# Performance work log

Hardware: AMD Instinct MI355X
Metric: run time of the kernel (lower is better)

The kernel has to match this reference:

```python
import jax, jax.numpy as jnp
import numpy as np

EPS_LN = 1e-6
EPS_STAT = 1e-10
EPS_BN = 1e-5


def _ln(x, g, b):
    mu = x.mean(-1, keepdims=True)
    var = x.var(-1, keepdims=True)
    return (x - mu) * jax.lax.rsqrt(var + EPS_LN) * g + b


def setup_inputs() -> dict:
    key = jax.random.key(0)
    ks = jax.random.split(key, 16)
    B, D, L, NB = 64, 256, 2048, 2
    H = 2 * D  # FFN inner dim
    s = 0.05   # small init scale for stability
    f32 = jnp.float32
    return {
        "x": jax.random.normal(ks[0], (B, D, L), f32),
        "wk": jax.random.normal(ks[1], (NB, 128, D), f32) * s,
        "wq": jax.random.normal(ks[2], (NB, 128, 2 * D), f32) * s,
        "fcq_w": jax.random.normal(ks[3], (NB, D, D), f32) * s,
        "fc_w": jax.random.normal(ks[4], (NB, D, 2 * D), f32) * s,
        "fc_b": jax.random.normal(ks[5], (NB, D), f32) * s,
        "att_ln_g": jnp.ones((NB, D), f32),
        "att_ln_b": jnp.zeros((NB, D), f32),
        "w1": jax.random.normal(ks[6], (NB, H, D), f32) * s,
        "b1": jax.random.normal(ks[7], (NB, H), f32) * s,
        "w2": jax.random.normal(ks[8], (NB, D, H), f32) * s,
        "b2": jax.random.normal(ks[9], (NB, D), f32) * s,
        "ffw_ln_g": jnp.ones((NB, D), f32),
        "ffw_ln_b": jnp.zeros((NB, D), f32),
    }


def reference(x, wk, wq, fcq_w, fc_w, fc_b, att_ln_g, att_ln_b,
              w1, b1, w2, b2, ffw_ln_g, ffw_ln_b):
    # x: (B, D, L)
    n_blocks = wk.shape[0]
    scale = 1.0 / np.sqrt(128.0)  # dim = k channel dim = 128
    v = x
    skip_sum = None
    for i in range(n_blocks):
        residual = v                                   # (B, D, L)
        vt = _ln(v.transpose(0, 2, 1), att_ln_g[i], att_ln_b[i])  # (B, L, D)
        k = jnp.einsum('bld,kd->blk', vt, wk[i])       # (B, L, 128)
        mu = vt.mean(axis=1, keepdims=True)            # (B, 1, D)
        sd = jnp.sqrt(jnp.clip(vt.var(axis=1, keepdims=True), EPS_STAT, None))
        q = jnp.einsum('bhe,ke->bhk',
                       jnp.concatenate([mu, sd], axis=2), wq[i])  # (B, 1, 128)
        scores = jnp.einsum('blk,bhk->bhl', k, q) * scale         # (B, 1, L)
        w = jax.nn.softmax(scores, axis=2)
        vdl = vt.transpose(0, 2, 1)                    # (B, D, L)
        att_mean = jnp.einsum('bdl,bhl->bdh', vdl, w)  # (B, D, 1)
        att_std = jnp.sqrt(jnp.clip(
            jnp.einsum('bdl,bhl->bdh', (vdl - att_mean) ** 2, w), EPS_STAT, None))
        skip = jnp.einsum('od,bdh->boh', fc_w[i],
                          jnp.concatenate([att_mean, att_std], axis=1)) \
               + fc_b[i][None, :, None]                # (B, D, 1)
        q_out = residual + jnp.einsum('od,bdh->boh', fcq_w[i], att_mean)  # (B, D, L)
        # PositionwiseFeedForward on (B, L, D)
        f_in = q_out.transpose(0, 2, 1)
        h = _ln(f_in, ffw_ln_g[i], ffw_ln_b[i])
        h1 = jax.nn.relu(jnp.einsum('bld,hd->blh', h, w1[i]) + b1[i])
        h2 = jnp.einsum('blh,dh->bld', h1, w2[i]) + b2[i]
        v = (h2 + f_in).transpose(0, 2, 1)             # (B, D, L)
        skip_sum = skip if skip_sum is None else skip_sum + skip
    # relu + BatchNorm1d (affine=False, training-mode batch stats)
    y = jax.nn.relu(skip_sum)                          # (B, D, 1)
    bm = y.mean(axis=(0, 2), keepdims=True)
    bv = y.var(axis=(0, 2), keepdims=True)
    return (y - bm) * jax.lax.rsqrt(bv + EPS_BN)
```

## Files before the change

kernel.cpp:

```cpp
#include <hip/hip_runtime.h>
#include <hip/hip_bf16.h>

#define DEV __device__ __forceinline__

constexpr int B = 64, D = 256, L = 2048, H = 512, KP = 128;
constexpr float EPS_LN = 1e-6f, EPS_STAT = 1e-10f, EPS_BN = 1e-5f;
constexpr float SCALE = 0.088388347648318447f;

typedef __attribute__((ext_vector_type(8))) short short8;
typedef __attribute__((ext_vector_type(4))) float float4_;
typedef __attribute__((ext_vector_type(2))) float float2_;

DEV unsigned short f2bf(float x) {
  unsigned u = __builtin_bit_cast(unsigned, x);
  u += 0x7fffu + ((u >> 16) & 1u);
  return (unsigned short)(u >> 16);
}

DEV unsigned pk2bf(float a, float b) {
  return (unsigned)f2bf(a) | ((unsigned)f2bf(b) << 16);
}

DEV float wred(float x) {
  #pragma unroll
  for (int o = 32; o > 0; o >>= 1) x += __shfl_down(x, o, 64);
  return x;
}
DEV float wredmax(float x) {
  #pragma unroll
  for (int o = 32; o > 0; o >>= 1) x = fmaxf(x, __shfl_down(x, o, 64));
  return x;
}

__global__ void k_convw(const float* __restrict__ w1, const float* __restrict__ w2,
                        unsigned short* __restrict__ w1b, unsigned short* __restrict__ w2b) {
  int n = H * D;
  for (int i = blockIdx.x * blockDim.x + threadIdx.x; i < n; i += gridDim.x * blockDim.x) {
    w1b[i] = f2bf(w1[i]);
    w2b[i] = f2bf(w2[i]);
  }
}

__global__ __launch_bounds__(512, 4) void k_pass1(
    const float* __restrict__ v, float* __restrict__ m, float* __restrict__ r,
    float* __restrict__ S1p, float* __restrict__ S2p) {
  __shared__ float ut[256 * 65];
  __shared__ float mu_s[64], rs_s[64];
  float* part1 = ut;
  float* part2 = ut + 2048;

  int blk = blockIdx.x;
  int b = blk >> 5, tile = blk & 31, l0 = tile * 64;
  int tid = threadIdx.x;
  int lane4 = tid & 15, rg = tid >> 4;

  const float* vrow = v + ((size_t)b * D + rg * 8) * L + l0 + lane4 * 4;
  float4_ vv[8];
  float4_ s1 = {0.f, 0.f, 0.f, 0.f}, s2 = {0.f, 0.f, 0.f, 0.f};
  #pragma unroll
  for (int j = 0; j < 8; ++j) {
    float4_ x = *(const float4_*)&vrow[(size_t)j * L];
    vv[j] = x; s1 += x; s2 += x * x;
  }
  #pragma unroll
  for (int c = 0; c < 4; ++c) {
    part1[rg * 64 + lane4 * 4 + c] = s1[c];
    part2[rg * 64 + lane4 * 4 + c] = s2[c];
  }
  __syncthreads();
  if (tid < 64) {
    float a = 0.f, c = 0.f;
    #pragma unroll
    for (int q = 0; q < 32; ++q) { a += part1[q * 64 + tid]; c += part2[q * 64 + tid]; }
    float mu = a * (1.f / D);
    float var = c * (1.f / D) - mu * mu;
    float rsq = rsqrtf(var + EPS_LN);
    mu_s[tid] = mu; rs_s[tid] = rsq;
    m[b * L + l0 + tid] = mu;
    r[b * L + l0 + tid] = rsq;
  }
  __syncthreads();
  {
    #pragma unroll
    for (int c = 0; c < 4; ++c) {
      int tok = lane4 * 4 + c;
      float mu = mu_s[tok], rsv = rs_s[tok];
      #pragma unroll
      for (int j = 0; j < 8; ++j)
        ut[(rg * 8 + j) * 65 + tok] = (vv[j][c] - mu) * rsv;
    }
  }
  __syncthreads();
  {
    int d = tid >> 1, hf = (tid & 1) * 32;
    float a1 = 0.f, a2 = 0.f;
    #pragma unroll
    for (int l2 = 0; l2 < 32; ++l2) {
      float u = ut[d * 65 + hf + l2];
      a1 += u; a2 += u * u;
    }
    a1 += __shfl_xor(a1, 1, 64);
    a2 += __shfl_xor(a2, 1, 64);
    if ((tid & 1) == 0) {
      S1p[((size_t)b * 32 + tile) * D + d] = a1;
      S2p[((size_t)b * 32 + tile) * D + d] = a2;
    }
  }
}

__global__ void k_qproj(const float* __restrict__ S1p, const float* __restrict__ S2p,
                        const float* __restrict__ g, const float* __restrict__ be,
                        const float* __restrict__ wq, const float* __restrict__ wk,
                        float* __restrict__ gw) {
  __shared__ float cat[2 * D];
  __shared__ float qs[KP];
  int b = blockIdx.x, t = threadIdx.x;
  {
    float s1 = 0.f, s2 = 0.f;
    for (int k = 0; k < 32; ++k) {
      s1 += S1p[((size_t)b * 32 + k) * D + t];
      s2 += S2p[((size_t)b * 32 + k) * D + t];
    }
    s1 *= (1.f / L); s2 *= (1.f / L);
    float gg = g[t];
    cat[t] = gg * s1 + be[t];
    float var = gg * gg * (s2 - s1 * s1);
    cat[D + t] = sqrtf(fmaxf(var, EPS_STAT));
  }
  __syncthreads();
  if (t < KP) {
    float s = 0.f;
    const float* wr = wq + t * 2 * D;
    for (int e = 0; e < 2 * D; ++e) s += cat[e] * wr[e];
    qs[t] = s;
  }
  __syncthreads();
  {
    float s = 0.f;
    for (int k = 0; k < KP; ++k) s += wk[k * D + t] * qs[k];
    gw[b * D + t] = g[t] * SCALE * s;
  }
}

__global__ void k_scores(const float* __restrict__ v, const float* __restrict__ m,
                         const float* __restrict__ r, const float* __restrict__ gw,
                         float* __restrict__ sc) {
  __shared__ float gws[D];
  int i2 = blockIdx.x * 256 + threadIdx.x;
  int b = i2 >> 10, l = (i2 & 1023) * 2;
  gws[threadIdx.x] = gw[b * D + threadIdx.x];
  __syncthreads();
  const float* p = v + (size_t)b * D * L + l;
  float2_ mm = *(const float2_*)&m[b * L + l];
  float2_ rr = *(const float2_*)&r[b * L + l];
  float2_ s = {0.f, 0.f};
  #pragma unroll 8
  for (int d = 0; d < D; ++d) {
    float2_ x = *(const float2_*)&p[(size_t)d * L];
    float g = gws[d];
    s += (x - mm) * g;
  }
  *(float2_*)&sc[b * L + l] = s * rr;
}

__global__ __launch_bounds__(256) void k_redw(
    const float* __restrict__ v, const float* __restrict__ m, const float* __restrict__ r,
    const float* __restrict__ sc, float* __restrict__ A1, float* __restrict__ A2) {
  __shared__ float ws[L];
  __shared__ float ms[L], rs[L];
  __shared__ float red[4];
  int blk = blockIdx.x;
  int b = blk >> 3, dt = (blk & 7) * 32;
  int tid = threadIdx.x, wv = tid >> 6, lane = tid & 63;

  float xc[8];
  float mx = -1e30f;
  #pragma unroll
  for (int k = 0; k < 8; ++k) {
    float x = sc[b * L + tid + k * 256];
    xc[k] = x; mx = fmaxf(mx, x);
  }
  mx = wredmax(mx);
  if (lane == 0) red[wv] = mx;
  __syncthreads();
  mx = fmaxf(fmaxf(red[0], red[1]), fmaxf(red[2], red[3]));
  float sm = 0.f;
  #pragma unroll
  for (int k = 0; k < 8; ++k) { float e = __expf(xc[k] - mx); xc[k] = e; sm += e; }
  sm = wred(sm);
  __syncthreads();
  if (lane == 0) red[wv] = sm;
  __syncthreads();
  float inv = 1.f / (red[0] + red[1] + red[2] + red[3]);
  #pragma unroll
  for (int k = 0; k < 8; ++k) ws[tid + k * 256] = xc[k] * inv;
  for (int l = tid; l < L; l += 256) { ms[l] = m[b * L + l]; rs[l] = r[b * L + l]; }
  __syncthreads();

  for (int j = 0; j < 8; ++j) {
    int d = dt + wv * 8 + j;
    const float* row = v + ((size_t)b * D + d) * L;
    float a1 = 0.f, a2 = 0.f;
    #pragma unroll
    for (int k2 = 0; k2 < 8; ++k2) {
      int l = lane * 4 + k2 * 256;
      float4_ x4 = *(const float4_*)&row[l];
      #pragma unroll
      for (int i = 0; i < 4; ++i) {
        float u = (x4[i] - ms[l + i]) * rs[l + i];
        float w = ws[l + i];
        a1 += w * u; a2 += w * u * u;
      }
    }
    a1 = wred(a1); a2 = wred(a2);
    if (lane == 0) { A1[b * D + d] = a1; A2[b * D + d] = a2; }
  }
}

__global__ void k_skip(const float* __restrict__ A1, const float* __restrict__ A2,
                       const float* __restrict__ g, const float* __restrict__ be,
                       const float* __restrict__ fcw, const float* __restrict__ fcb,
                       const float* __restrict__ fcqw,
                       float* __restrict__ skip_i, float* __restrict__ fcq) {
  __shared__ float am[D], as_[D];
  int b = blockIdx.x, t = threadIdx.x;
  {
    float a1 = A1[b * D + t], a2 = A2[b * D + t], gg = g[t];
    am[t] = gg * a1 + be[t];
    float var = gg * gg * (a2 - a1 * a1);
    as_[t] = sqrtf(fmaxf(var, EPS_STAT));
  }
  __syncthreads();
  float s = fcb[t], fq = 0.f;
  const float* wr = fcw + t * 2 * D;
  const float* qr = fcqw + t * D;
  for (int d = 0; d < D; ++d) {
    s += wr[d] * am[d] + wr[D + d] * as_[d];
    fq += qr[d] * am[d];
  }
  skip_i[b * D + t] = s;
  fcq[b * D + t] = fq;
}

constexpr int MT = 64;

#define GEMM1_HALF(H0, ACC)                                                          \
  {                                                                                  \
    const unsigned short* wp0 = w1b + (size_t)((H0) + lr) * D + lq * 8;              \
    const unsigned short* wp1 = wp0 + 16 * D;                                        \
    short8 wr0[8], wr1[8];                                                           \
    _Pragma("unroll")                                                                \
    for (int kk = 0; kk < 8; ++kk) {                                                 \
      wr0[kk] = *(const short8*)(wp0 + kk * 32);                                     \
      wr1[kk] = *(const short8*)(wp1 + kk * 32);                                     \
    }                                                                                \
    int abase = lq * 512 + lr * 8;                                                   \
    _Pragma("unroll")                                                                \
    for (int kk = 0; kk < 8; ++kk) {                                                 \
      int nb = abase + kk * 2048;                                                    \
      short8 bf0 = *(const short8*)&us[nb];                                          \
      short8 bf1 = *(const short8*)&us[nb + 128];                                    \
      short8 bf2 = *(const short8*)&us[nb + 256];                                    \
      short8 bf3 = *(const short8*)&us[nb + 384];                                    \
      ACC[0][0] = __builtin_amdgcn_mfma_f32_16x16x32_bf16(wr0[kk], bf0, ACC[0][0],0,0,0);\
      ACC[0][1] = __builtin_amdgcn_mfma_f32_16x16x32_bf16(wr0[kk], bf1, ACC[0][1],0,0,0);\
      ACC[0][2] = __builtin_amdgcn_mfma_f32_16x16x32_bf16(wr0[kk], bf2, ACC[0][2],0,0,0);\
      ACC[0][3] = __builtin_amdgcn_mfma_f32_16x16x32_bf16(wr0[kk], bf3, ACC[0][3],0,0,0);\
      ACC[1][0] = __builtin_amdgcn_mfma_f32_16x16x32_bf16(wr1[kk], bf0, ACC[1][0],0,0,0);\
      ACC[1][1] = __builtin_amdgcn_mfma_f32_16x16x32_bf16(wr1[kk], bf1, ACC[1][1],0,0,0);\
      ACC[1][2] = __builtin_amdgcn_mfma_f32_16x16x32_bf16(wr1[kk], bf2, ACC[1][2],0,0,0);\
      ACC[1][3] = __builtin_amdgcn_mfma_f32_16x16x32_bf16(wr1[kk], bf3, ACC[1][3],0,0,0);\
    }                                                                                \
  }

#define H1_WRITE(H0, ACC)                                                            \
  {                                                                                  \
    _Pragma("unroll")                                                                \
    for (int mh = 0; mh < 2; ++mh) {                                                 \
      int hb = (H0) + mh * 16 + lq * 4;                                              \
      float b10 = b1[hb], b11 = b1[hb + 1], b12 = b1[hb + 2], b13 = b1[hb + 3];      \
      int grp = ((hb >> 3) + 32) & 63;                                               \
      int jh0 = hb & 7;                                                              \
      _Pragma("unroll")                                                              \
      for (int nt = 0; nt < 4; ++nt) {                                               \
        int tok = nt * 16 + lr;                                                      \
        uint2 pk;                                                                    \
        pk.x = pk2bf(fmaxf(ACC[mh][nt][0] + b10, 0.f),                               \
                     fmaxf(ACC[mh][nt][1] + b11, 0.f));                              \
        pk.y = pk2bf(fmaxf(ACC[mh][nt][2] + b12, 0.f),                               \
                     fmaxf(ACC[mh][nt][3] + b13, 0.f));                              \
        *(uint2*)&us[grp * 512 + tok * 8 + jh0] = pk;                                \
      }                                                                              \
    }                                                                                \
  }

#define GEMM2_HALF(M0, ACC2)                                                         \
  {                                                                                  \
    const unsigned short* wp = w2b + (size_t)((M0) + lr) * H + lq * 8;               \
    short8 wrg[16];                                                                  \
    _Pragma("unroll")                                                                \
    for (int kk = 0; kk < 16; ++kk) wrg[kk] = *(const short8*)(wp + kk * 32);        \
    _Pragma("unroll")                                                                \
    for (int kk = 0; kk < 16; ++kk) {                                                \
      int hb = ((kk * 4 + lq + 32) & 63) * 512 + lr * 8;                             \
      short8 hf0 = *(const short8*)&us[hb];                                          \
      short8 hf1 = *(const short8*)&us[hb + 128];                                    \
      short8 hf2 = *(const short8*)&us[hb + 256];                                    \
      short8 hf3 = *(const short8*)&us[hb + 384];                                    \
      ACC2[0] = __builtin_amdgcn_mfma_f32_16x16x32_bf16(wrg[kk], hf0, ACC2[0], 0, 0, 0);\
      ACC2[1] = __builtin_amdgcn_mfma_f32_16x16x32_bf16(wrg[kk], hf1, ACC2[1], 0, 0, 0);\
      ACC2[2] = __builtin_amdgcn_mfma_f32_16x16x32_bf16(wrg[kk], hf2, ACC2[2], 0, 0, 0);\
      ACC2[3] = __builtin_amdgcn_mfma_f32_16x16x32_bf16(wrg[kk], hf3, ACC2[3], 0, 0, 0);\
    }                                                                                \
  }

#define EPI_HALF(M0, ACC2)                                                           \
  {                                                                                  \
    _Pragma("unroll")                                                                \
    for (int i = 0; i < 4; ++i) {                                                    \
      int d = (M0) + lq * 4 + i;                                                     \
      float bb = b2_s[d] + fcq_s[d];                                                 \
      size_t rowoff = ((size_t)b * D + d) * L + l0;                                  \
      _Pragma("unroll")                                                              \
      for (int nt = 0; nt < 4; ++nt) {                                               \
        int tok = nt * 16 + lr;                                                      \
        dst[rowoff + tok] = ACC2[nt][i] + bb + src[rowoff + tok];                    \
      }                                                                              \
    }                                                                                \
  }

__global__ __launch_bounds__(512, 4) void k_ffn(
    const float* src, float* dst, const float* __restrict__ fcq,
    const unsigned short* __restrict__ w1b, const float* __restrict__ b1,
    const unsigned short* __restrict__ w2b, const float* __restrict__ b2,
    const float* __restrict__ g, const float* __restrict__ be) {
  __shared__ __align__(16) unsigned short us[32768];
  __shared__ float fcq_s[D], g_s[D], be_s[D], b2_s[D];
  __shared__ __align__(16) float mu_s[MT], rs_s[MT];
  float* part1 = (float*)us;
  float* part2 = (float*)(us + 4096);

  int blk = blockIdx.x;
  int b = blk >> 5;
  int l0 = (blk & 31) * MT;
  int tid = threadIdx.x;
  int lane4 = tid & 15, rg = tid >> 4;
  int wv = tid >> 6, lane = tid & 63, lr = lane & 15, lq = lane >> 4;

  if (tid < D) {
    fcq_s[tid] = fcq[b * D + tid];
    g_s[tid] = g[tid]; be_s[tid] = be[tid]; b2_s[tid] = b2[tid];
  }
  __syncthreads();

  const float* vrow = src + ((size_t)b * D + rg * 8) * L + l0 + lane4 * 4;
  float4_ vv[8];
  float4_ s1 = {0.f, 0.f, 0.f, 0.f}, s2 = {0.f, 0.f, 0.f, 0.f};
  #pragma unroll
  for (int j = 0; j < 8; ++j) {
    float4_ x = *(const float4_*)&vrow[(size_t)j * L];
    x = x + fcq_s[rg * 8 + j];
    vv[j] = x; s1 += x; s2 += x * x;
  }
  *(float4_*)&part1[rg * 64 + lane4 * 4] = s1;
  *(float4_*)&part2[rg * 64 + lane4 * 4] = s2;
  __syncthreads();
  if (tid < MT) {
    float a = 0.f, c = 0.f;
    #pragma unroll
    for (int q = 0; q < 32; ++q) { a += part1[q * 64 + tid]; c += part2[q * 64 + tid]; }
    float mu = a * (1.f / D);
    float var = c * (1.f / D) - mu * mu;
    mu_s[tid] = mu; rs_s[tid] = rsqrtf(var + EPS_LN);
  }
  __syncthreads();
  {
    float4_ mu4 = *(const float4_*)&mu_s[lane4 * 4];
    float4_ rs4 = *(const float4_*)&rs_s[lane4 * 4];
    #pragma unroll
    for (int c = 0; c < 4; ++c) {
      uint4 pw;
      unsigned* pp = &pw.x;
      #pragma unroll
      for (int jj = 0; jj < 4; ++jj) {
        int d0 = rg * 8 + jj * 2;
        pp[jj] = pk2bf((vv[jj * 2][c]     - mu4[c]) * rs4[c] * g_s[d0]     + be_s[d0],
                       (vv[jj * 2 + 1][c] - mu4[c]) * rs4[c] * g_s[d0 + 1] + be_s[d0 + 1]);
      }
      *(uint4*)&us[(rg * 64 + lane4 * 4 + c) * 8] = pw;
    }
  }
  __syncthreads();

  float4_ zero = {0.f, 0.f, 0.f, 0.f};

  {
    float4_ accA[2][4];
    #pragma unroll
    for (int i = 0; i < 2; ++i)
      #pragma unroll
      for (int j = 0; j < 4; ++j) accA[i][j] = zero;
    GEMM1_HALF(wv * 32, accA)
    H1_WRITE(wv * 32, accA)
  }
  {
    float4_ accB[2][4];
    #pragma unroll
    for (int i = 0; i < 2; ++i)
      #pragma unroll
      for (int j = 0; j < 4; ++j) accB[i][j] = zero;
    GEMM1_HALF(256 + wv * 32, accB)
    __syncthreads();
    H1_WRITE(256 + wv * 32, accB)
  }
  __syncthreads();

  {
    float4_ acc2[4];
    #pragma unroll
    for (int j = 0; j < 4; ++j) acc2[j] = zero;
    GEMM2_HALF(wv * 16, acc2)
    EPI_HALF(wv * 16, acc2)
  }
  {
    float4_ acc2[4];
    #pragma unroll
    for (int j = 0; j < 4; ++j) acc2[j] = zero;
    GEMM2_HALF(128 + wv * 16, acc2)
    EPI_HALF(128 + wv * 16, acc2)
  }
}

__global__ void k_bn(const float* __restrict__ s0, const float* __restrict__ s1,
                     float* __restrict__ out) {
  int d = threadIdx.x;
  float s = 0.f, q = 0.f;
  for (int b = 0; b < B; ++b) {
    float y = fmaxf(s0[b * D + d] + s1[b * D + d], 0.f);
    s += y; q += y * y;
  }
  float mu = s * (1.f / B);
  float var = q * (1.f / B) - mu * mu;
  float rs = rsqrtf(var + EPS_BN);
  for (int b = 0; b < B; ++b) {
    float y = fmaxf(s0[b * D + d] + s1[b * D + d], 0.f);
    out[b * D + d] = (y - mu) * rs;
  }
}

extern "C" void kernel_launch(void* const* d_in, const int* in_sizes, int n_in,
                              void* d_out, int out_size, void* d_ws, size_t ws_size,
                              hipStream_t stream) {
  const float* x    = (const float*)d_in[0];
  const float* wk   = (const float*)d_in[1];
  const float* wq   = (const float*)d_in[2];
  const float* fcqw = (const float*)d_in[3];
  const float* fcw  = (const float*)d_in[4];
  const float* fcb  = (const float*)d_in[5];
  const float* ag   = (const float*)d_in[6];
  const float* abt  = (const float*)d_in[7];
  const float* w1   = (const float*)d_in[8];
  const float* b1   = (const float*)d_in[9];
  const float* w2   = (const float*)d_in[10];
  const float* b2   = (const float*)d_in[11];
  const float* fg   = (const float*)d_in[12];
  const float* fb   = (const float*)d_in[13];
  float* out = (float*)d_out;

  char* p = (char*)d_ws;
  float* v_ws = (float*)p;  p += (size_t)B * D * L * 4;
  float* m    = (float*)p;  p += (size_t)B * L * 4;
  float* r    = (float*)p;  p += (size_t)B * L * 4;
  float* sc   = (float*)p;  p += (size_t)B * L * 4;
  float* S1p  = (float*)p;  p += (size_t)B * 32 * D * 4;
  float* S2p  = (float*)p;  p += (size_t)B * 32 * D * 4;
  float* gw   = (float*)p;  p += (size_t)B * D * 4;
  float* A1   = (float*)p;  p += (size_t)B * D * 4;
  float* A2   = (float*)p;  p += (size_t)B * D * 4;
  float* fcqv = (float*)p;  p += (size_t)B * D * 4;
  float* sk0  = (float*)p;  p += (size_t)B * D * 4;
  float* sk1  = (float*)p;  p += (size_t)B * D * 4;
  unsigned short* w1b = (unsigned short*)p; p += (size_t)H * D * 2;
  unsigned short* w2b = (unsigned short*)p; p += (size_t)D * H * 2;

  k_convw<<<256, 256, 0, stream>>>(w1, w2, w1b, w2b);

  for (int i = 0; i < 2; ++i) {
    const float* src = (i == 0) ? x : v_ws;
    k_pass1<<<B * 32, 512, 0, stream>>>(src, m, r, S1p, S2p);
    k_qproj<<<B, 256, 0, stream>>>(S1p, S2p, ag + i * D, abt + i * D,
                                   wq + (size_t)i * KP * 2 * D,
                                   wk + (size_t)i * KP * D, gw);
    k_scores<<<B * L / 512, 256, 0, stream>>>(src, m, r, gw, sc);
    k_redw<<<B * 8, 256, 0, stream>>>(src, m, r, sc, A1, A2);
    k_skip<<<B, 256, 0, stream>>>(A1, A2, ag + i * D, abt + i * D,
                                  fcw + (size_t)i * D * 2 * D, fcb + i * D,
                                  fcqw + (size_t)i * D * D,
                                  (i == 0) ? sk0 : sk1, fcqv);
    if (i == 0) {
      k_ffn<<<B * (L / MT), 512, 0, stream>>>(src, v_ws, fcqv,
                                              w1b, b1, w2b, b2, fg, fb);
    }
  }
  k_bn<<<1, 256, 0, stream>>>(sk0, sk1, out);
}
```

Baseline: 619.4 us.

## Streamline stats pass, split score reduction over channels, and widen redw grid

The per-tile channel statistics in pass1 are now computed straight from registers with lane shuffles, which removes the large transposed shared-memory tile and a barrier, so occupancy can rise. The score kernel factors the mean subtraction out algebraically: qproj precomputes the sum of gw per batch, so scores become r*(dot - m*G). Scores also split the channel sum across two halves of a 512-thread block, one token per thread. The weighted-reduction kernel now uses twice as many blocks with fewer channels each, which adds parallelism but makes each block recompute the softmax redundantly.

```diff
diff --git a/kernel.cpp b/kernel.cpp
--- a/kernel.cpp
+++ b/kernel.cpp
@@ -9,7 +9,6 @@
 
 typedef __attribute__((ext_vector_type(8))) short short8;
 typedef __attribute__((ext_vector_type(4))) float float4_;
-typedef __attribute__((ext_vector_type(2))) float float2_;
 
 DEV unsigned short f2bf(float x) {
   unsigned u = __builtin_bit_cast(unsigned, x);
@@ -44,10 +43,8 @@
 __global__ __launch_bounds__(512, 4) void k_pass1(
     const float* __restrict__ v, float* __restrict__ m, float* __restrict__ r,
     float* __restrict__ S1p, float* __restrict__ S2p) {
-  __shared__ float ut[256 * 65];
-  __shared__ float mu_s[64], rs_s[64];
-  float* part1 = ut;
-  float* part2 = ut + 2048;
+  __shared__ float part1[32 * 64], part2[32 * 64];
+  __shared__ __align__(16) float mu_s[64], rs_s[64];
 
   int blk = blockIdx.x;
   int b = blk >> 5, tile = blk & 31, l0 = tile * 64;
@@ -62,11 +59,8 @@
     float4_ x = *(const float4_*)&vrow[(size_t)j * L];
     vv[j] = x; s1 += x; s2 += x * x;
   }
-  #pragma unroll
-  for (int c = 0; c < 4; ++c) {
-    part1[rg * 64 + lane4 * 4 + c] = s1[c];
-    part2[rg * 64 + lane4 * 4 + c] = s2[c];
-  }
+  *(float4_*)&part1[rg * 64 + lane4 * 4] = s1;
+  *(float4_*)&part2[rg * 64 + lane4 * 4] = s2;
   __syncthreads();
   if (tid < 64) {
     float a = 0.f, c = 0.f;
@@ -81,29 +75,20 @@
   }
   __syncthreads();
   {
-    #pragma unroll
-    for (int c = 0; c < 4; ++c) {
-      int tok = lane4 * 4 + c;
-      float mu = mu_s[tok], rsv = rs_s[tok];
+    float4_ mu4 = *(const float4_*)&mu_s[lane4 * 4];
+    float4_ rs4 = *(const float4_*)&rs_s[lane4 * 4];
+    size_t obase = ((size_t)b * 32 + tile) * D + rg * 8;
+    #pragma unroll
+    for (int j = 0; j < 8; ++j) {
+      float4_ u = (vv[j] - mu4) * rs4;
+      float a1 = u[0] + u[1] + u[2] + u[3];
+      float a2 = u[0] * u[0] + u[1] * u[1] + u[2] * u[2] + u[3] * u[3];
       #pragma unroll
-      for (int j = 0; j < 8; ++j)
-        ut[(rg * 8 + j) * 65 + tok] = (vv[j][c] - mu) * rsv;
-    }
-  }
-  __syncthreads();
-  {
-    int d = tid >> 1, hf = (tid & 1) * 32;
-    float a1 = 0.f, a2 = 0.f;
-    #pragma unroll
-    for (int l2 = 0; l2 < 32; ++l2) {
-      float u = ut[d * 65 + hf + l2];
-      a1 += u; a2 += u * u;
-    }
-    a1 += __shfl_xor(a1, 1, 64);
-    a2 += __shfl_xor(a2, 1, 64);
-    if ((tid & 1) == 0) {
-      S1p[((size_t)b * 32 + tile) * D + d] = a1;
-      S2p[((size_t)b * 32 + tile) * D + d] = a2;
+      for (int o = 1; o < 16; o <<= 1) {
+        a1 += __shfl_xor(a1, o, 64);
+        a2 += __shfl_xor(a2, o, 64);
+      }
+      if (lane4 == 0) { S1p[obase + j] = a1; S2p[obase + j] = a2; }
     }
   }
 }
@@ -111,9 +96,10 @@
 __global__ void k_qproj(const float* __restrict__ S1p, const float* __restrict__ S2p,
                         const float* __restrict__ g, const float* __restrict__ be,
                         const float* __restrict__ wq, const float* __restrict__ wk,
-                        float* __restrict__ gw) {
+                        float* __restrict__ gw, float* __restrict__ Gg) {
   __shared__ float cat[2 * D];
   __shared__ float qs[KP];
+  __shared__ float gsum[4];
   int b = blockIdx.x, t = threadIdx.x;
   {
     float s1 = 0.f, s2 = 0.f;
@@ -138,29 +124,37 @@
   {
     float s = 0.f;
     for (int k = 0; k < KP; ++k) s += wk[k * D + t] * qs[k];
-    gw[b * D + t] = g[t] * SCALE * s;
-  }
-}
-
-__global__ void k_scores(const float* __restrict__ v, const float* __restrict__ m,
-                         const float* __restrict__ r, const float* __restrict__ gw,
-                         float* __restrict__ sc) {
+    float gwv = g[t] * SCALE * s;
+    gw[b * D + t] = gwv;
+    float gs = wred(gwv);
+    if ((t & 63) == 0) gsum[t >> 6] = gs;
+  }
+  __syncthreads();
+  if (t == 0) Gg[b] = gsum[0] + gsum[1] + gsum[2] + gsum[3];
+}
+
+__global__ __launch_bounds__(512) void k_scores(
+    const float* __restrict__ v, const float* __restrict__ m,
+    const float* __restrict__ r, const float* __restrict__ gw,
+    const float* __restrict__ Gg, float* __restrict__ sc) {
   __shared__ float gws[D];
-  int i2 = blockIdx.x * 256 + threadIdx.x;
-  int b = i2 >> 10, l = (i2 & 1023) * 2;
-  gws[threadIdx.x] = gw[b * D + threadIdx.x];
-  __syncthreads();
-  const float* p = v + (size_t)b * D * L + l;
-  float2_ mm = *(const float2_*)&m[b * L + l];
-  float2_ rr = *(const float2_*)&r[b * L + l];
-  float2_ s = {0.f, 0.f};
+  __shared__ float sh[256];
+  int blk = blockIdx.x;
+  int b = blk >> 3, l0 = (blk & 7) * 256;
+  int tid = threadIdx.x, lt = tid & 255, dh = tid >> 8;
+  if (tid < D) gws[tid] = gw[b * D + tid];
+  __syncthreads();
+  int l = l0 + lt;
+  const float* p = v + ((size_t)b * D + dh * 128) * L + l;
+  float s = 0.f;
   #pragma unroll 8
-  for (int d = 0; d < D; ++d) {
-    float2_ x = *(const float2_*)&p[(size_t)d * L];
-    float g = gws[d];
-    s += (x - mm) * g;
-  }
-  *(float2_*)&sc[b * L + l] = s * rr;
+  for (int d = 0; d < 128; ++d) s += p[(size_t)d * L] * gws[dh * 128 + d];
+  if (dh == 1) sh[lt] = s;
+  __syncthreads();
+  if (dh == 0) {
+    float tot = s + sh[lt];
+    sc[b * L + l] = r[b * L + l] * (tot - m[b * L + l] * Gg[b]);
+  }
 }
 
 __global__ __launch_bounds__(256) void k_redw(
@@ -170,7 +164,7 @@
   __shared__ float ms[L], rs[L];
   __shared__ float red[4];
   int blk = blockIdx.x;
-  int b = blk >> 3, dt = (blk & 7) * 32;
+  int b = blk >> 4, dt = (blk & 15) * 16;
   int tid = threadIdx.x, wv = tid >> 6, lane = tid & 63;
 
   float xc[8];
@@ -197,8 +191,8 @@
   for (int l = tid; l < L; l += 256) { ms[l] = m[b * L + l]; rs[l] = r[b * L + l]; }
   __syncthreads();
 
-  for (int j = 0; j < 8; ++j) {
-    int d = dt + wv * 8 + j;
+  for (int j = 0; j < 4; ++j) {
+    int d = dt + wv * 4 + j;
     const float* row = v + ((size_t)b * D + d) * L;
     float a1 = 0.f, a2 = 0.f;
     #pragma unroll
@@ -480,6 +474,7 @@
   float* fcqv = (float*)p;  p += (size_t)B * D * 4;
   float* sk0  = (float*)p;  p += (size_t)B * D * 4;
   float* sk1  = (float*)p;  p += (size_t)B * D * 4;
+  float* Gg   = (float*)p;  p += (size_t)B * 4;
   unsigned short* w1b = (unsigned short*)p; p += (size_t)H * D * 2;
   unsigned short* w2b = (unsigned short*)p; p += (size_t)D * H * 2;
 
@@ -490,9 +485,9 @@
     k_pass1<<<B * 32, 512, 0, stream>>>(src, m, r, S1p, S2p);
     k_qproj<<<B, 256, 0, stream>>>(S1p, S2p, ag + i * D, abt + i * D,
                                    wq + (size_t)i * KP * 2 * D,
-                                   wk + (size_t)i * KP * D, gw);
-    k_scores<<<B * L / 512, 256, 0, stream>>>(src, m, r, gw, sc);
-    k_redw<<<B * 8, 256, 0, stream>>>(src, m, r, sc, A1, A2);
+                                   wk + (size_t)i * KP * D, gw, Gg);
+    k_scores<<<B * 8, 512, 0, stream>>>(src, m, r, gw, Gg, sc);
+    k_redw<<<B * 16, 256, 0, stream>>>(src, m, r, sc, A1, A2);
     k_skip<<<B, 256, 0, stream>>>(A1, A2, ag + i * D, abt + i * D,
                                   fcw + (size_t)i * D * 2 * D, fcb + i * D,
                                   fcqw + (size_t)i * D * D,
```

New measurement: 599.4 us. 3.2% less time.
